# Performance work log

Hardware: AMD Instinct MI355X
Metric: run time of the kernel (lower is better)

The kernel has to match this reference:

```python
import jax, jax.numpy as jnp
import numpy as np

N_NODES = 100000   # total atoms across batch
N_EDGES = 1600000  # directed edges (avg degree 16)
ATOM_FDIM = 75
N_MOLS = 1024
DEPTH = 3


def setup_inputs() -> dict:
    key = jax.random.key(0)
    ks = jax.random.split(key, 8)
    h = jax.random.normal(ks[0], (N_NODES, ATOM_FDIM), dtype=jnp.float32)
    # U: Linear(2*atom_fdim -> atom_fdim); NN: Linear(atom_fdim -> 1)
    U_w = jax.random.normal(ks[1], (ATOM_FDIM, 2 * ATOM_FDIM), dtype=jnp.float32) * (1.0 / np.sqrt(2 * ATOM_FDIM))
    U_b = jnp.zeros((ATOM_FDIM,), dtype=jnp.float32)
    NN_w = jax.random.normal(ks[2], (1, ATOM_FDIM), dtype=jnp.float32) * (1.0 / np.sqrt(ATOM_FDIM))
    NN_b = jnp.zeros((1,), dtype=jnp.float32)
    edge_src = jax.random.randint(ks[3], (N_EDGES,), 0, N_NODES, dtype=jnp.int32)
    edge_dst = jax.random.randint(ks[4], (N_EDGES,), 0, N_NODES, dtype=jnp.int32)
    mol_id = jnp.sort(jax.random.randint(ks[5], (N_NODES,), 0, N_MOLS, dtype=jnp.int32))
    return {
        "h": h, "U_w": U_w, "U_b": U_b, "NN_w": NN_w, "NN_b": NN_b,
        "edge_src": edge_src, "edge_dst": edge_dst, "mol_id": mol_id,
        "depth": DEPTH, "num_mols": N_MOLS,
    }


def reference(h, U_w, U_b, NN_w, NN_b, edge_src, edge_dst, mol_id, depth, num_mols):
    n_nodes = h.shape[0]
    for _ in range(depth):
        # message: sum of neighbor atom features (gather + scatter-add)
        m = jax.ops.segment_sum(h[edge_src], edge_dst, num_segments=n_nodes)  # [N, D]
        # update: h_v = relu(U([h_v ; m_v]))
        h = jax.nn.relu(jnp.concatenate([h, m], axis=-1) @ U_w.T + U_b)
    # readout: sum atom vectors per molecule, then Linear(D -> 1)
    mol_vec = jax.ops.segment_sum(h, mol_id, num_segments=num_mols)  # [B, D]
    out = mol_vec @ NN_w.T + NN_b  # [B, 1]
    return out
```

## Files before the change

kernel.cpp:

```cpp
#include <hip/hip_runtime.h>

#define FDIM 75
#define CDIM 150
#define NSB 80
#define BW 7
#define BSZ (1 << BW)
#define TILE_E 4096
#define EPT 16

typedef __attribute__((ext_vector_type(8))) short bf16x8;
typedef __attribute__((ext_vector_type(4))) float f32x4;
typedef __attribute__((ext_vector_type(4))) int   i32x4;

__device__ __forceinline__ unsigned f2bf(float x) {
    unsigned u = __float_as_uint(x);
    return (u + 0x7FFFu + ((u >> 16) & 1u)) >> 16;
}
__device__ __forceinline__ float bf_lo(unsigned u) { return __uint_as_float(u << 16); }
__device__ __forceinline__ float bf_hi(unsigned u) { return __uint_as_float(u & 0xFFFF0000u); }

__global__ void pad_convert_kernel(const float* __restrict__ h_in,
                                   unsigned* __restrict__ h40, int n_nodes) {
    int i = blockIdx.x * blockDim.x + threadIdx.x;
    int total = n_nodes * 40;
    if (i >= total) return;
    int v = i / 40, d = i - v * 40;
    int f0 = 2 * d, f1 = 2 * d + 1;
    float a = (f0 < FDIM) ? h_in[(size_t)v * FDIM + f0] : 0.0f;
    float b = (f1 < FDIM) ? h_in[(size_t)v * FDIM + f1] : 0.0f;
    h40[i] = f2bf(a) | (f2bf(b) << 16);
}

__global__ void wprep_kernel(const float* __restrict__ Uw,
                             unsigned short* __restrict__ wpack) {
    int i = blockIdx.x * blockDim.x + threadIdx.x;
    if (i >= 1600) return;
    int kb = i / 80, c = i - kb * 80;
    unsigned short out[8];
#pragma unroll
    for (int j = 0; j < 8; ++j) {
        int k = kb * 8 + j;
        float v = 0.0f;
        if (c < FDIM) {
            if (k < FDIM)                 v = Uw[(size_t)c * CDIM + k];
            else if (k >= 80 && k < 155)  v = Uw[(size_t)c * CDIM + FDIM + (k - 80)];
        }
        out[j] = (unsigned short)f2bf(v);
    }
    *(i32x4*)&wpack[(size_t)i * 8] = *(i32x4*)out;
}

__global__ __launch_bounds__(256) void bcount_kernel(
        const int* __restrict__ edst, int* __restrict__ bcnt,
        int n_edges, int nb) {
    __shared__ int lh[1024];
    int tid = threadIdx.x;
    for (int i = tid; i < nb; i += 256) lh[i] = 0;
    __syncthreads();
    for (int e = blockIdx.x * blockDim.x + tid; e < n_edges;
         e += gridDim.x * blockDim.x)
        atomicAdd(&lh[edst[e] >> BW], 1);
    __syncthreads();
    for (int i = tid; i < nb; i += 256)
        if (lh[i]) atomicAdd(&bcnt[i], lh[i]);
}

__global__ __launch_bounds__(1024) void bscan_kernel(
        const int* __restrict__ bcnt, int* __restrict__ bbase,
        int* __restrict__ gcur, int* __restrict__ row_ptr,
        int nb, int n_nodes) {
    __shared__ int s[1024];
    int t = threadIdx.x;
    int v = (t < nb) ? bcnt[t] : 0;
    s[t] = v;
    __syncthreads();
    for (int off = 1; off < 1024; off <<= 1) {
        int x = (t >= off) ? s[t - off] : 0;
        __syncthreads();
        s[t] += x;
        __syncthreads();
    }
    if (t < nb) {
        int ex = s[t] - v;
        bbase[t] = ex;
        gcur[t] = ex;
    }
    if (t == nb - 1) {
        bbase[nb] = s[t];
        row_ptr[n_nodes] = s[t];
    }
}

__global__ __launch_bounds__(256) void bpart_kernel(
        const int* __restrict__ esrc, const int* __restrict__ edst,
        int* __restrict__ gcur, unsigned* __restrict__ pairs,
        int n_edges, int nb) {
    __shared__ int lh[1024];
    __shared__ int tbase[1024];
    int tid = threadIdx.x;
    int base = blockIdx.x * TILE_E;
    unsigned packedR[EPT];
    int bR[EPT];
    for (int i = tid; i < nb; i += 256) lh[i] = 0;
    __syncthreads();
#pragma unroll
    for (int k = 0; k < EPT; ++k) {
        int e = base + k * 256 + tid;
        if (e < n_edges) {
            int d = edst[e];
            int s = esrc[e];
            bR[k] = d >> BW;
            packedR[k] = ((unsigned)(d & (BSZ - 1)) << 17) | (unsigned)s;
            atomicAdd(&lh[bR[k]], 1);
        } else {
            bR[k] = -1;
        }
    }
    __syncthreads();
    for (int i = tid; i < nb; i += 256) {
        int c = lh[i];
        if (c) tbase[i] = atomicAdd(&gcur[i], c);
        lh[i] = 0;
    }
    __syncthreads();
#pragma unroll
    for (int k = 0; k < EPT; ++k) {
        if (bR[k] >= 0) {
            int off = atomicAdd(&lh[bR[k]], 1);
            pairs[tbase[bR[k]] + off] = packedR[k];
        }
    }
}

__global__ __launch_bounds__(256) void bfill_kernel(
        const unsigned* __restrict__ pairs, const int* __restrict__ bbase,
        int* __restrict__ row_ptr, int* __restrict__ csr, int n_nodes) {
    __shared__ int cnt[BSZ];
    __shared__ int ofs[BSZ];
    __shared__ int cur[BSZ];
    int b = blockIdx.x;
    int tid = threadIdx.x;
    int v0 = b << BW;
    int nbk = n_nodes - v0;
    if (nbk > BSZ) nbk = BSZ;
    int sbeg = bbase[b];
    int ne = bbase[b + 1] - sbeg;
    if (tid < BSZ) { cnt[tid] = 0; cur[tid] = 0; }
    __syncthreads();
    for (int i = tid; i < ne; i += 256)
        atomicAdd(&cnt[pairs[sbeg + i] >> 17], 1);
    __syncthreads();
    if (tid < BSZ) ofs[tid] = cnt[tid];
    __syncthreads();
    for (int off = 1; off < BSZ; off <<= 1) {
        int x = 0;
        if (tid < BSZ && tid >= off) x = ofs[tid - off];
        __syncthreads();
        if (tid < BSZ) ofs[tid] += x;
        __syncthreads();
    }
    if (tid < nbk) row_ptr[v0 + tid] = sbeg + ofs[tid] - cnt[tid];
    __syncthreads();
    for (int i = tid; i < ne; i += 256) {
        unsigned p = pairs[sbeg + i];
        int dl = p >> 17;
        int src = p & 0x1FFFF;
        int pos = (ofs[dl] - cnt[dl]) + atomicAdd(&cur[dl], 1);
        csr[sbeg + pos] = src;
    }
}

#define LOAD8(myi, dd, A0, A1, C0, C1)                                   \
    {                                                                     \
        int s0 = __shfl(myi, dd + 0), s1 = __shfl(myi, dd + 1);           \
        int s2 = __shfl(myi, dd + 2), s3 = __shfl(myi, dd + 3);           \
        int s4 = __shfl(myi, dd + 4), s5 = __shfl(myi, dd + 5);           \
        int s6 = __shfl(myi, dd + 6), s7 = __shfl(myi, dd + 7);           \
        if (act) {                                                        \
            unsigned u0 = h32[(size_t)s0 * 40 + lane];                    \
            unsigned u1 = h32[(size_t)s1 * 40 + lane];                    \
            unsigned u2 = h32[(size_t)s2 * 40 + lane];                    \
            unsigned u3 = h32[(size_t)s3 * 40 + lane];                    \
            unsigned u4 = h32[(size_t)s4 * 40 + lane];                    \
            unsigned u5 = h32[(size_t)s5 * 40 + lane];                    \
            unsigned u6 = h32[(size_t)s6 * 40 + lane];                    \
            unsigned u7 = h32[(size_t)s7 * 40 + lane];                    \
            A0 += bf_lo(u0); C0 += bf_hi(u0);                             \
            A1 += bf_lo(u1); C1 += bf_hi(u1);                             \
            A0 += bf_lo(u2); C0 += bf_hi(u2);                             \
            A1 += bf_lo(u3); C1 += bf_hi(u3);                             \
            A0 += bf_lo(u4); C0 += bf_hi(u4);                             \
            A1 += bf_lo(u5); C1 += bf_hi(u5);                             \
            A0 += bf_lo(u6); C0 += bf_hi(u6);                             \
            A1 += bf_lo(u7); C1 += bf_hi(u7);                             \
        }                                                                 \
    }

__global__ __launch_bounds__(256) void gather_kernel(
        const unsigned* __restrict__ h32, unsigned* __restrict__ m32,
        const int* __restrict__ row_ptr, const int* __restrict__ csr,
        int n_nodes) {
    int lane = threadIdx.x & 63;
    int wid = blockIdx.x * (blockDim.x >> 6) + (threadIdx.x >> 6);
    int nwaves = gridDim.x * (blockDim.x >> 6);
    bool act = (lane < 40);

    for (int v0 = wid * 2; v0 < n_nodes; v0 += nwaves * 2) {
        int vA = v0;
        int vB = v0 + 1;
        bool hasB = (vB < n_nodes);
        int eA = row_ptr[vA], e1A = row_ptr[vA + 1];
        int eB = hasB ? row_ptr[vB] : 0;
        int e1B = hasB ? row_ptr[vB + 1] : 0;
        float aA0 = 0.f, aA1 = 0.f, cA0 = 0.f, cA1 = 0.f;
        float aB0 = 0.f, aB1 = 0.f, cB0 = 0.f, cB1 = 0.f;

        while (eA < e1A || eB < e1B) {
            int cntA = e1A - eA; if (cntA > 64) cntA = 64; if (cntA < 0) cntA = 0;
            int cntB = e1B - eB; if (cntB > 64) cntB = 64; if (cntB < 0) cntB = 0;
            int myiA = (lane < cntA) ? csr[eA + lane] : 0;
            int myiB = (lane < cntB) ? csr[eB + lane] : 0;
            int dA = 0, dB = 0;
            while (dA + 8 <= cntA && dB + 8 <= cntB) {
                LOAD8(myiA, dA, aA0, aA1, cA0, cA1);
                LOAD8(myiB, dB, aB0, aB1, cB0, cB1);
                dA += 8; dB += 8;
            }
            while (dA + 8 <= cntA) { LOAD8(myiA, dA, aA0, aA1, cA0, cA1); dA += 8; }
            while (dB + 8 <= cntB) { LOAD8(myiB, dB, aB0, aB1, cB0, cB1); dB += 8; }
            for (; dA + 4 <= cntA; dA += 4) {
                int s0 = __shfl(myiA, dA + 0), s1 = __shfl(myiA, dA + 1);
                int s2 = __shfl(myiA, dA + 2), s3 = __shfl(myiA, dA + 3);
                if (act) {
                    unsigned u0 = h32[(size_t)s0 * 40 + lane];
                    unsigned u1 = h32[(size_t)s1 * 40 + lane];
                    unsigned u2 = h32[(size_t)s2 * 40 + lane];
                    unsigned u3 = h32[(size_t)s3 * 40 + lane];
                    aA0 += bf_lo(u0); cA0 += bf_hi(u0);
                    aA1 += bf_lo(u1); cA1 += bf_hi(u1);
                    aA0 += bf_lo(u2); cA0 += bf_hi(u2);
                    aA1 += bf_lo(u3); cA1 += bf_hi(u3);
                }
            }
            for (; dB + 4 <= cntB; dB += 4) {
                int s0 = __shfl(myiB, dB + 0), s1 = __shfl(myiB, dB + 1);
                int s2 = __shfl(myiB, dB + 2), s3 = __shfl(myiB, dB + 3);
                if (act) {
                    unsigned u0 = h32[(size_t)s0 * 40 + lane];
                    unsigned u1 = h32[(size_t)s1 * 40 + lane];
                    unsigned u2 = h32[(size_t)s2 * 40 + lane];
                    unsigned u3 = h32[(size_t)s3 * 40 + lane];
                    aB0 += bf_lo(u0); cB0 += bf_hi(u0);
                    aB1 += bf_lo(u1); cB1 += bf_hi(u1);
                    aB0 += bf_lo(u2); cB0 += bf_hi(u2);
                    aB1 += bf_lo(u3); cB1 += bf_hi(u3);
                }
            }
            for (; dA < cntA; ++dA) {
                int s0 = __shfl(myiA, dA);
                if (act) {
                    unsigned u0 = h32[(size_t)s0 * 40 + lane];
                    aA0 += bf_lo(u0); cA0 += bf_hi(u0);
                }
            }
            for (; dB < cntB; ++dB) {
                int s0 = __shfl(myiB, dB);
                if (act) {
                    unsigned u0 = h32[(size_t)s0 * 40 + lane];
                    aB0 += bf_lo(u0); cB0 += bf_hi(u0);
                }
            }
            eA += cntA; eB += cntB;
        }
        if (act) {
            float lo = aA0 + aA1, hi = cA0 + cA1;
            m32[(size_t)vA * 40 + lane] = f2bf(lo) | (f2bf(hi) << 16);
            if (hasB) {
                lo = aB0 + aB1; hi = cB0 + cB1;
                m32[(size_t)vB * 40 + lane] = f2bf(lo) | (f2bf(hi) << 16);
            }
        }
    }
}

__global__ __launch_bounds__(256) void update_mfma_kernel(
        unsigned short* __restrict__ h, const unsigned short* __restrict__ m,
        const unsigned short* __restrict__ wpack, const float* __restrict__ Ub,
        int n_nodes) {
    __shared__ __align__(16) unsigned short Xl[4][16][168];
    int tid = threadIdx.x;

    int base = blockIdx.x * 64;
    for (int i = tid; i < 64 * 20; i += 256) {
        int nl = i / 20, p = i - nl * 20;
        int v = base + nl;
        i32x4 val = {0, 0, 0, 0};
        if (v < n_nodes) {
            const unsigned short* src = (p < 10)
                ? h + (size_t)v * NSB + p * 8
                : m + (size_t)v * NSB + (p - 10) * 8;
            val = *(const i32x4*)src;
        }
        *(i32x4*)&Xl[nl >> 4][nl & 15][p * 8] = val;
    }
    __syncthreads();

    int w = tid >> 6;
    int lane = tid & 63;
    int col = lane & 15;
    int kb = lane >> 4;

    f32x4 acc[5] = {};
#pragma unroll
    for (int t = 0; t < 5; ++t) {
        bf16x8 a = *(bf16x8*)&Xl[w][col][t * 32 + kb * 8];
#pragma unroll
        for (int jt = 0; jt < 5; ++jt) {
            bf16x8 b = *(const bf16x8*)&wpack[((size_t)((t * 4 + kb) * 80 + jt * 16 + col)) * 8];
            acc[jt] = __builtin_amdgcn_mfma_f32_16x16x32_bf16(a, b, acc[jt], 0, 0, 0);
        }
    }

#pragma unroll
    for (int jt = 0; jt < 5; ++jt) {
        int c = jt * 16 + col;
        float bj = (c < FDIM) ? Ub[c] : 0.0f;
#pragma unroll
        for (int r = 0; r < 4; ++r) {
            int node = base + w * 16 + kb * 4 + r;
            if (node < n_nodes) {
                float vv = fmaxf(acc[jt][r] + bj, 0.0f);
                h[(size_t)node * NSB + c] = (unsigned short)f2bf(vv);
            }
        }
    }
}

__global__ __launch_bounds__(256) void readout_mol_kernel(
        const unsigned* __restrict__ h32, const float* __restrict__ NNw,
        const int* __restrict__ mol_id, const float* __restrict__ NN_b,
        float* __restrict__ out, int n_nodes) {
    int b = blockIdx.x;
    int lo = 0, hi = n_nodes;
    while (lo < hi) {
        int mid = (lo + hi) >> 1;
        if (mol_id[mid] < b) lo = mid + 1; else hi = mid;
    }
    int start = lo;
    hi = n_nodes;
    while (lo < hi) {
        int mid = (lo + hi) >> 1;
        if (mol_id[mid] < b + 1) lo = mid + 1; else hi = mid;
    }
    int end = lo;

    int tid = threadIdx.x;
    int wave = tid >> 6, lane = tid & 63;
    float w0 = 0.f, w1 = 0.f;
    if (lane < 40) {
        w0 = (2 * lane < FDIM) ? NNw[2 * lane] : 0.f;
        w1 = (2 * lane + 1 < FDIM) ? NNw[2 * lane + 1] : 0.f;
    }
    float wsum = 0.f;
    for (int v = start + wave; v < end; v += 4) {
        if (lane < 40) {
            unsigned u = h32[(size_t)v * 40 + lane];
            wsum += bf_lo(u) * w0 + bf_hi(u) * w1;
        }
    }
    wsum += __shfl_down(wsum, 32);
    wsum += __shfl_down(wsum, 16);
    wsum += __shfl_down(wsum, 8);
    wsum += __shfl_down(wsum, 4);
    wsum += __shfl_down(wsum, 2);
    wsum += __shfl_down(wsum, 1);
    __shared__ float part[4];
    if (lane == 0) part[wave] = wsum;
    __syncthreads();
    if (tid == 0) out[b] = NN_b[0] + part[0] + part[1] + part[2] + part[3];
}

extern "C" void kernel_launch(void* const* d_in, const int* in_sizes, int n_in,
                              void* d_out, int out_size, void* d_ws, size_t ws_size,
                              hipStream_t stream) {
    const float* h_src = (const float*)d_in[0];
    const float* U_w   = (const float*)d_in[1];
    const float* U_b   = (const float*)d_in[2];
    const float* NN_w  = (const float*)d_in[3];
    const float* NN_b  = (const float*)d_in[4];
    const int*   esrc  = (const int*)d_in[5];
    const int*   edst  = (const int*)d_in[6];
    const int*   molid = (const int*)d_in[7];

    int n_nodes  = in_sizes[0] / FDIM;
    int n_edges  = in_sizes[5];
    int num_mols = out_size;
    const int depth = 3;
    int nb = (n_nodes + BSZ - 1) >> BW;

    size_t row_bytes = (size_t)n_nodes * NSB * sizeof(unsigned short);

    size_t off = 0;
    auto alloc = [&](size_t bytes) {
        size_t o = off;
        off += (bytes + 255) & ~(size_t)255;
        return o;
    };
    char* ws = (char*)d_ws;
    size_t o_h     = alloc(row_bytes);
    size_t o_m     = alloc(row_bytes);
    size_t o_rp    = alloc(((size_t)n_nodes + 1) * sizeof(int));
    size_t o_csr   = alloc((size_t)n_edges * sizeof(int));
    size_t o_wp    = alloc(12800 * sizeof(unsigned short));
    size_t o_bcnt  = alloc((size_t)(nb + 1) * sizeof(int));
    size_t o_bbase = alloc((size_t)(nb + 1) * sizeof(int));
    size_t o_gcur  = alloc((size_t)(nb + 1) * sizeof(int));
    (void)ws_size;

    float* out = (float*)d_out;
    unsigned short* h = (unsigned short*)(ws + o_h);
    unsigned short* m = (unsigned short*)(ws + o_m);
    unsigned* pairs = (unsigned*)(ws + o_m);
    int* row_ptr = (int*)(ws + o_rp);
    int* csr     = (int*)(ws + o_csr);
    unsigned short* wpack = (unsigned short*)(ws + o_wp);
    int* bcnt    = (int*)(ws + o_bcnt);
    int* bbase   = (int*)(ws + o_bbase);
    int* gcur    = (int*)(ws + o_gcur);

    pad_convert_kernel<<<(n_nodes * 40 + 255) / 256, 256, 0, stream>>>(
        h_src, (unsigned*)h, n_nodes);
    wprep_kernel<<<7, 256, 0, stream>>>(U_w, wpack);

    hipMemsetAsync(bcnt, 0, (size_t)nb * sizeof(int), stream);
    bcount_kernel<<<256, 256, 0, stream>>>(edst, bcnt, n_edges, nb);
    bscan_kernel<<<1, 1024, 0, stream>>>(bcnt, bbase, gcur, row_ptr, nb, n_nodes);
    bpart_kernel<<<(n_edges + TILE_E - 1) / TILE_E, 256, 0, stream>>>(
        esrc, edst, gcur, pairs, n_edges, nb);
    bfill_kernel<<<nb, 256, 0, stream>>>(pairs, bbase, row_ptr, csr, n_nodes);

    int ublocks = (n_nodes + 63) / 64;
    for (int d = 0; d < depth; ++d) {
        gather_kernel<<<2048, 256, 0, stream>>>(
            (const unsigned*)h, (unsigned*)m, row_ptr, csr, n_nodes);
        update_mfma_kernel<<<ublocks, 256, 0, stream>>>(h, m, wpack, U_b, n_nodes);
    }

    readout_mol_kernel<<<num_mols, 256, 0, stream>>>(
        (const unsigned*)h, NN_w, molid, NN_b, out, n_nodes);
}
```

Baseline: 288.9 us.

## Fuse readout into final update kernel and merge setup kernels

Merges padding/conversion, weight packing and bucket-count zeroing into one pre-kernel, and initializes the output with the bias inside the scan kernel. The final update kernel now computes per-node dot products with NN_w directly from the MFMA accumulators, runs a segmented scan by molecule id within the block, and atomically adds to the output. This removes the separate readout kernel with its binary searches and the last write/read of h, at the cost of float atomics that make summation order nondeterministic.

```diff
diff --git a/kernel.cpp b/kernel.cpp
--- a/kernel.cpp
+++ b/kernel.cpp
@@ -19,35 +19,37 @@
 __device__ __forceinline__ float bf_lo(unsigned u) { return __uint_as_float(u << 16); }
 __device__ __forceinline__ float bf_hi(unsigned u) { return __uint_as_float(u & 0xFFFF0000u); }
 
-__global__ void pad_convert_kernel(const float* __restrict__ h_in,
-                                   unsigned* __restrict__ h40, int n_nodes) {
-    int i = blockIdx.x * blockDim.x + threadIdx.x;
+__global__ void pre_kernel(const float* __restrict__ h_in,
+                           unsigned* __restrict__ h40,
+                           const float* __restrict__ Uw,
+                           unsigned short* __restrict__ wpack,
+                           int* __restrict__ bcnt,
+                           int n_nodes, int nb) {
+    int gid = blockIdx.x * blockDim.x + threadIdx.x;
     int total = n_nodes * 40;
-    if (i >= total) return;
-    int v = i / 40, d = i - v * 40;
-    int f0 = 2 * d, f1 = 2 * d + 1;
-    float a = (f0 < FDIM) ? h_in[(size_t)v * FDIM + f0] : 0.0f;
-    float b = (f1 < FDIM) ? h_in[(size_t)v * FDIM + f1] : 0.0f;
-    h40[i] = f2bf(a) | (f2bf(b) << 16);
-}
-
-__global__ void wprep_kernel(const float* __restrict__ Uw,
-                             unsigned short* __restrict__ wpack) {
-    int i = blockIdx.x * blockDim.x + threadIdx.x;
-    if (i >= 1600) return;
-    int kb = i / 80, c = i - kb * 80;
-    unsigned short out[8];
-#pragma unroll
-    for (int j = 0; j < 8; ++j) {
-        int k = kb * 8 + j;
-        float v = 0.0f;
-        if (c < FDIM) {
-            if (k < FDIM)                 v = Uw[(size_t)c * CDIM + k];
-            else if (k >= 80 && k < 155)  v = Uw[(size_t)c * CDIM + FDIM + (k - 80)];
-        }
-        out[j] = (unsigned short)f2bf(v);
-    }
-    *(i32x4*)&wpack[(size_t)i * 8] = *(i32x4*)out;
+    if (gid < total) {
+        int v = gid / 40, d = gid - v * 40;
+        int f0 = 2 * d, f1 = 2 * d + 1;
+        float a = (f0 < FDIM) ? h_in[(size_t)v * FDIM + f0] : 0.0f;
+        float b = (f1 < FDIM) ? h_in[(size_t)v * FDIM + f1] : 0.0f;
+        h40[gid] = f2bf(a) | (f2bf(b) << 16);
+    }
+    if (gid < 1600) {
+        int kb = gid / 80, c = gid - kb * 80;
+        unsigned short outw[8];
+#pragma unroll
+        for (int j = 0; j < 8; ++j) {
+            int k = kb * 8 + j;
+            float v = 0.0f;
+            if (c < FDIM) {
+                if (k < FDIM)                 v = Uw[(size_t)c * CDIM + k];
+                else if (k >= 80 && k < 155)  v = Uw[(size_t)c * CDIM + FDIM + (k - 80)];
+            }
+            outw[j] = (unsigned short)f2bf(v);
+        }
+        *(i32x4*)&wpack[(size_t)gid * 8] = *(i32x4*)outw;
+    }
+    if (gid >= 2048 && gid < 2048 + nb + 1) bcnt[gid - 2048] = 0;
 }
 
 __global__ __launch_bounds__(256) void bcount_kernel(
@@ -68,9 +70,11 @@
 __global__ __launch_bounds__(1024) void bscan_kernel(
         const int* __restrict__ bcnt, int* __restrict__ bbase,
         int* __restrict__ gcur, int* __restrict__ row_ptr,
-        int nb, int n_nodes) {
+        int nb, int n_nodes,
+        float* __restrict__ out, const float* __restrict__ NN_b, int num_mols) {
     __shared__ int s[1024];
     int t = threadIdx.x;
+    if (t < num_mols) out[t] = NN_b[0];
     int v = (t < nb) ? bcnt[t] : 0;
     s[t] = v;
     __syncthreads();
@@ -283,11 +287,14 @@
     }
 }
 
+template <int LAST>
 __global__ __launch_bounds__(256) void update_mfma_kernel(
         unsigned short* __restrict__ h, const unsigned short* __restrict__ m,
         const unsigned short* __restrict__ wpack, const float* __restrict__ Ub,
-        int n_nodes) {
+        const float* __restrict__ NNw, const int* __restrict__ mol_id,
+        float* __restrict__ out, int n_nodes) {
     __shared__ __align__(16) unsigned short Xl[4][16][168];
+    __shared__ float pernode[64];
     int tid = threadIdx.x;
 
     int base = blockIdx.x * 64;
@@ -321,63 +328,67 @@
         }
     }
 
+    float bj[5], wj[5];
 #pragma unroll
     for (int jt = 0; jt < 5; ++jt) {
         int c = jt * 16 + col;
-        float bj = (c < FDIM) ? Ub[c] : 0.0f;
+        bj[jt] = (c < FDIM) ? Ub[c] : 0.0f;
+        if (LAST) wj[jt] = (c < FDIM) ? NNw[c] : 0.0f;
+    }
+
+    if (!LAST) {
+#pragma unroll
+        for (int jt = 0; jt < 5; ++jt) {
+            int c = jt * 16 + col;
+#pragma unroll
+            for (int r = 0; r < 4; ++r) {
+                int node = base + w * 16 + kb * 4 + r;
+                if (node < n_nodes) {
+                    float vv = fmaxf(acc[jt][r] + bj[jt], 0.0f);
+                    h[(size_t)node * NSB + c] = (unsigned short)f2bf(vv);
+                }
+            }
+        }
+    } else {
+        float pd[4];
 #pragma unroll
         for (int r = 0; r < 4; ++r) {
-            int node = base + w * 16 + kb * 4 + r;
-            if (node < n_nodes) {
-                float vv = fmaxf(acc[jt][r] + bj, 0.0f);
-                h[(size_t)node * NSB + c] = (unsigned short)f2bf(vv);
-            }
-        }
-    }
-}
-
-__global__ __launch_bounds__(256) void readout_mol_kernel(
-        const unsigned* __restrict__ h32, const float* __restrict__ NNw,
-        const int* __restrict__ mol_id, const float* __restrict__ NN_b,
-        float* __restrict__ out, int n_nodes) {
-    int b = blockIdx.x;
-    int lo = 0, hi = n_nodes;
-    while (lo < hi) {
-        int mid = (lo + hi) >> 1;
-        if (mol_id[mid] < b) lo = mid + 1; else hi = mid;
-    }
-    int start = lo;
-    hi = n_nodes;
-    while (lo < hi) {
-        int mid = (lo + hi) >> 1;
-        if (mol_id[mid] < b + 1) lo = mid + 1; else hi = mid;
-    }
-    int end = lo;
-
-    int tid = threadIdx.x;
-    int wave = tid >> 6, lane = tid & 63;
-    float w0 = 0.f, w1 = 0.f;
-    if (lane < 40) {
-        w0 = (2 * lane < FDIM) ? NNw[2 * lane] : 0.f;
-        w1 = (2 * lane + 1 < FDIM) ? NNw[2 * lane + 1] : 0.f;
-    }
-    float wsum = 0.f;
-    for (int v = start + wave; v < end; v += 4) {
-        if (lane < 40) {
-            unsigned u = h32[(size_t)v * 40 + lane];
-            wsum += bf_lo(u) * w0 + bf_hi(u) * w1;
-        }
-    }
-    wsum += __shfl_down(wsum, 32);
-    wsum += __shfl_down(wsum, 16);
-    wsum += __shfl_down(wsum, 8);
-    wsum += __shfl_down(wsum, 4);
-    wsum += __shfl_down(wsum, 2);
-    wsum += __shfl_down(wsum, 1);
-    __shared__ float part[4];
-    if (lane == 0) part[wave] = wsum;
-    __syncthreads();
-    if (tid == 0) out[b] = NN_b[0] + part[0] + part[1] + part[2] + part[3];
+            float s = 0.0f;
+#pragma unroll
+            for (int jt = 0; jt < 5; ++jt)
+                s += fmaxf(acc[jt][r] + bj[jt], 0.0f) * wj[jt];
+            pd[r] = s;
+        }
+#pragma unroll
+        for (int r = 0; r < 4; ++r) {
+            pd[r] += __shfl_xor(pd[r], 1, 16);
+            pd[r] += __shfl_xor(pd[r], 2, 16);
+            pd[r] += __shfl_xor(pd[r], 4, 16);
+            pd[r] += __shfl_xor(pd[r], 8, 16);
+        }
+        if (col == 0) {
+#pragma unroll
+            for (int r = 0; r < 4; ++r)
+                pernode[w * 16 + kb * 4 + r] = pd[r];
+        }
+        __syncthreads();
+        if (tid < 64) {
+            int node = base + tid;
+            bool valid = (node < n_nodes);
+            float val = valid ? pernode[tid] : 0.0f;
+            int mol = valid ? mol_id[node] : 0x7FFFFFFF;
+#pragma unroll
+            for (int off = 1; off < 64; off <<= 1) {
+                float vo = __shfl_up(val, off);
+                int mo = __shfl_up(mol, off);
+                if (tid >= off && mo == mol) val += vo;
+            }
+            int nm = __shfl_down(mol, 1);
+            bool tail = (tid == 63) || (nm != mol);
+            if (tail && mol != 0x7FFFFFFF)
+                unsafeAtomicAdd(&out[mol], val);
+        }
+    }
 }
 
 extern "C" void kernel_launch(void* const* d_in, const int* in_sizes, int n_in,
@@ -428,13 +439,12 @@
     int* bbase   = (int*)(ws + o_bbase);
     int* gcur    = (int*)(ws + o_gcur);
 
-    pad_convert_kernel<<<(n_nodes * 40 + 255) / 256, 256, 0, stream>>>(
-        h_src, (unsigned*)h, n_nodes);
-    wprep_kernel<<<7, 256, 0, stream>>>(U_w, wpack);
-
-    hipMemsetAsync(bcnt, 0, (size_t)nb * sizeof(int), stream);
+    pre_kernel<<<(n_nodes * 40 + 255) / 256, 256, 0, stream>>>(
+        h_src, (unsigned*)h, U_w, wpack, bcnt, n_nodes, nb);
+
     bcount_kernel<<<256, 256, 0, stream>>>(edst, bcnt, n_edges, nb);
-    bscan_kernel<<<1, 1024, 0, stream>>>(bcnt, bbase, gcur, row_ptr, nb, n_nodes);
+    bscan_kernel<<<1, 1024, 0, stream>>>(bcnt, bbase, gcur, row_ptr, nb, n_nodes,
+                                         out, NN_b, num_mols);
     bpart_kernel<<<(n_edges + TILE_E - 1) / TILE_E, 256, 0, stream>>>(
         esrc, edst, gcur, pairs, n_edges, nb);
     bfill_kernel<<<nb, 256, 0, stream>>>(pairs, bbase, row_ptr, csr, n_nodes);
@@ -443,9 +453,12 @@
     for (int d = 0; d < depth; ++d) {
         gather_kernel<<<2048, 256, 0, stream>>>(
             (const unsigned*)h, (unsigned*)m, row_ptr, csr, n_nodes);
-        update_mfma_kernel<<<ublocks, 256, 0, stream>>>(h, m, wpack, U_b, n_nodes);
-    }
-
-    readout_mol_kernel<<<num_mols, 256, 0, stream>>>(
-        (const unsigned*)h, NN_w, molid, NN_b, out, n_nodes);
-}
+        if (d < depth - 1) {
+            update_mfma_kernel<0><<<ublocks, 256, 0, stream>>>(
+                h, m, wpack, U_b, NN_w, molid, out, n_nodes);
+        } else {
+            update_mfma_kernel<1><<<ublocks, 256, 0, stream>>>(
+                h, m, wpack, U_b, NN_w, molid, out, n_nodes);
+        }
+    }
+}
```

New measurement: 259.5 us. 1.11x faster.
